# Kernel tuning notes

Measured on AMD Instinct MI355X. Metric: run time of the kernel, lower is better.

Reference implementation:

```python
import jax, jax.numpy as jnp
import numpy as np

EPS = 1e-10
BETA_SCALE = 1.0
TEMP = 0.5


def setup_inputs() -> dict:
    key = jax.random.key(0)
    ks = jax.random.split(key, 8)
    D = 128
    return {
        "root_mu_min": jax.random.normal(ks[0], (1, 64, D), dtype=jnp.float32),
        "root_mu_max": jax.random.normal(ks[1], (1, 64, D), dtype=jnp.float32),
        "root_beta_min_raw": jax.random.normal(ks[2], (1, 64, D), dtype=jnp.float32),
        "root_beta_max_raw": jax.random.normal(ks[3], (1, 64, D), dtype=jnp.float32),
        "adj_logits0": jax.random.normal(ks[4], (512, 64), dtype=jnp.float32),
        "adj_logits1": jax.random.normal(ks[5], (2048, 512), dtype=jnp.float32),
        "u0": jax.random.uniform(ks[6], (1, 512, 64), dtype=jnp.float32),
        "u1": jax.random.uniform(ks[7], (1, 2048, 512), dtype=jnp.float32),
    }


def _gumbel_sigmoid_hard(logits, u):
    # gumbel noise from externally supplied uniforms, straight-through hard threshold
    g = -jnp.log(-jnp.log(u + EPS) + EPS)
    y_soft = jax.nn.sigmoid((logits + g) / TEMP)
    y_hard = (y_soft > 0.5).astype(y_soft.dtype)
    return y_hard - jax.lax.stop_gradient(y_soft) + y_soft


def _weighted_intersection(mu_min, mu_max, beta_min, beta_max, w):
    # w: (1, C, P); parent boxes: (1, P, D)
    wsum = jnp.sum(w, axis=2)[..., None] + EPS                      # (1, C, 1)
    b_min = jnp.einsum('bcp,bpd->bcd', w, beta_min) / wsum           # (1, C, D)
    b_max = jnp.einsum('bcp,bpd->bcd', w, beta_max) / wsum           # (1, C, D)
    logw = jnp.log(w + EPS)[..., None]                               # (1, C, P, 1)
    arg_min = logw + mu_min[:, None, :, :] / b_min[:, :, None, :]    # (1, C, P, D)
    mu_min_i = b_min * jax.nn.logsumexp(arg_min, axis=2)             # (1, C, D)
    arg_max = logw - mu_max[:, None, :, :] / b_max[:, :, None, :]    # (1, C, P, D)
    mu_max_i = -b_max * jax.nn.logsumexp(arg_max, axis=2)            # (1, C, D)
    return mu_min_i, mu_max_i, b_min, b_max


def reference(root_mu_min, root_mu_max, root_beta_min_raw, root_beta_max_raw,
              adj_logits0, adj_logits1, u0, u1):
    beta_min = jax.nn.sigmoid(root_beta_min_raw) * BETA_SCALE + 1e-6
    beta_max = jax.nn.sigmoid(root_beta_max_raw) * BETA_SCALE + 1e-6
    level = (root_mu_min, root_mu_max, beta_min, beta_max)
    outs = list(level)
    for logits, u in ((adj_logits0, u0), (adj_logits1, u1)):
        w = _gumbel_sigmoid_hard(logits[None], u)  # (1, C, P)
        level = _weighted_intersection(*level, w)
        outs.extend(level)
    return tuple(outs)
```

## Files before the change

kernel.cpp:

```cpp
#include <hip/hip_runtime.h>
#include <cmath>

#define DD 128
#define LOG2E 1.4426950408889634f
#define MMARGIN 4.16f

__device__ __forceinline__ float sigm(float x) { return 1.0f / (1.0f + __expf(-x)); }

__global__ __launch_bounds__(512, 4)
void k_lvl1(const float* __restrict__ mu_min0, const float* __restrict__ mu_max0,
            const float* __restrict__ braw_min, const float* __restrict__ braw_max,
            const float* __restrict__ adj0, const float* __restrict__ u0,
            float* __restrict__ out,
            float2* __restrict__ mu2_1, float2* __restrict__ bb2_1,
            float4* __restrict__ pmaxf) {
    __shared__ float wsh[64];
    __shared__ int npres;
    __shared__ float4 red[8][64];
    __shared__ float4 cmx[8][64];
    __shared__ float4 carrA[64], carrB[64];
    const int tid = threadIdx.x;
    const int w = tid >> 6, lane = tid & 63;
    const int c = blockIdx.x;

    if (tid < 16) {
        int i = blockIdx.x * 16 + tid;
        out[i] = mu_min0[i];
        out[8192 + i] = mu_max0[i];
        out[16384 + i] = sigm(braw_min[i]) + 1e-6f;
        out[24576 + i] = sigm(braw_max[i]) + 1e-6f;
    }

    if (tid < 64) {
        int idx = c * 64 + tid;
        float uu = u0[idx] + 1e-10f;
        float g = -__logf(-__logf(uu) + 1e-10f);
        bool pres = (adj0[idx] + g) > 0.0f;
        wsh[tid] = pres ? 1.0f : 1e-10f;
        unsigned long long m = __ballot(pres);
        if (tid == 0) npres = (int)__popcll(m);
    }
    __syncthreads();

    const int p0 = w * 8;
    const int dbase = 2 * lane;

    float4 accB = make_float4(0.f, 0.f, 0.f, 0.f);
    float4 mrow[8];
    float wreg[8];
    float cm_mn0 = -INFINITY, cm_mn1 = -INFINITY, cm_ng0 = -INFINITY, cm_ng1 = -INFINITY;
    #pragma unroll
    for (int z = 0; z < 8; ++z) {
        int p = p0 + z;
        float2 bmr = *(const float2*)(braw_min + p * DD + dbase);
        float2 bxr = *(const float2*)(braw_max + p * DD + dbase);
        float2 mnr = *(const float2*)(mu_min0 + p * DD + dbase);
        float2 mxr = *(const float2*)(mu_max0 + p * DD + dbase);
        float bm0 = sigm(bmr.x) + 1e-6f, bm1 = sigm(bmr.y) + 1e-6f;
        float bx0 = sigm(bxr.x) + 1e-6f, bx1 = sigm(bxr.y) + 1e-6f;
        mrow[z] = make_float4(mnr.x, mxr.x, mnr.y, mxr.y);
        cm_mn0 = fmaxf(cm_mn0, mnr.x); cm_mn1 = fmaxf(cm_mn1, mnr.y);
        cm_ng0 = fmaxf(cm_ng0, -mxr.x); cm_ng1 = fmaxf(cm_ng1, -mxr.y);
        float wv = wsh[p];
        wreg[z] = wv;
        accB.x = fmaf(wv, bm0, accB.x);
        accB.y = fmaf(wv, bx0, accB.y);
        accB.z = fmaf(wv, bm1, accB.z);
        accB.w = fmaf(wv, bx1, accB.w);
    }
    red[w][lane] = accB;
    cmx[w][lane] = make_float4(cm_mn0, cm_ng0, cm_mn1, cm_ng1);
    __syncthreads();

    float bmin0, bmax0, bmin1, bmax1, rmin0, rmin1, nrmax0, nrmax1, Mm0, Mm1, Mg0, Mg1;
    if (tid < 64) {
        float4 S = red[0][lane];
        float4 M = cmx[0][lane];
        #pragma unroll
        for (int ww = 1; ww < 8; ++ww) {
            float4 t = red[ww][lane];
            S.x += t.x; S.y += t.y; S.z += t.z; S.w += t.w;
            float4 m = cmx[ww][lane];
            M.x = fmaxf(M.x, m.x); M.y = fmaxf(M.y, m.y);
            M.z = fmaxf(M.z, m.z); M.w = fmaxf(M.w, m.w);
        }
        Mm0 = M.x; Mg0 = M.y; Mm1 = M.z; Mg1 = M.w;
        if (c == 0) {
            pmaxf[lane] = make_float4(Mm0 + MMARGIN, Mg0 + MMARGIN,
                                      Mm1 + MMARGIN, Mg1 + MMARGIN);
        }
        const float wsv = (float)npres + 1e-10f;
        bmin0 = S.x / wsv; bmax0 = S.y / wsv; bmin1 = S.z / wsv; bmax1 = S.w / wsv;
        rmin0 = 1.0f / fmaxf(bmin0, 1e-30f);
        rmin1 = 1.0f / fmaxf(bmin1, 1e-30f);
        nrmax0 = -1.0f / fmaxf(bmax0, 1e-30f);
        nrmax1 = -1.0f / fmaxf(bmax1, 1e-30f);
        float rm20 = rmin0 * LOG2E, rm21 = rmin1 * LOG2E;
        float nx20 = nrmax0 * LOG2E, nx21 = nrmax1 * LOG2E;
        carrA[lane] = make_float4(rm20, rm21, nx20, nx21);
        carrB[lane] = make_float4(-rm20 * Mm0, -rm21 * Mm1, nx20 * Mg0, nx21 * Mg1);
    }
    __syncthreads();

    float4 cA = carrA[lane], cB = carrB[lane];

    float4 accS = make_float4(0.f, 0.f, 0.f, 0.f);
    #pragma unroll
    for (int z = 0; z < 8; ++z) {
        float4 q = mrow[z];
        float wv = wreg[z];
        accS.x = fmaf(wv, __builtin_amdgcn_exp2f(fmaf(q.x, cA.x, cB.x)), accS.x);
        accS.y = fmaf(wv, __builtin_amdgcn_exp2f(fmaf(q.y, cA.z, cB.z)), accS.y);
        accS.z = fmaf(wv, __builtin_amdgcn_exp2f(fmaf(q.z, cA.y, cB.y)), accS.z);
        accS.w = fmaf(wv, __builtin_amdgcn_exp2f(fmaf(q.w, cA.w, cB.w)), accS.w);
    }
    red[w][lane] = accS;
    __syncthreads();

    if (tid < 64) {
        float4 S = red[0][lane];
        #pragma unroll
        for (int ww = 1; ww < 8; ++ww) {
            float4 t = red[ww][lane];
            S.x += t.x; S.y += t.y; S.z += t.z; S.w += t.w;
        }
        const float S10 = fmaxf(S.x, 1e-35f);
        const float S20 = fmaxf(S.y, 1e-35f);
        const float S11 = fmaxf(S.z, 1e-35f);
        const float S21 = fmaxf(S.w, 1e-35f);
        const int idx = c * DD + 2 * lane;
        float v10 = bmin0 * fmaf(rmin0, Mm0, __logf(S10));
        float v11 = bmin1 * fmaf(rmin1, Mm1, __logf(S11));
        float v20 = -bmax0 * fmaf(-nrmax0, Mg0, __logf(S20));
        float v21 = -bmax1 * fmaf(-nrmax1, Mg1, __logf(S21));
        *(float2*)(out + 32768 + idx)  = make_float2(v10, v11);
        *(float2*)(out + 98304 + idx)  = make_float2(v20, v21);
        *(float2*)(out + 163840 + idx) = make_float2(bmin0, bmin1);
        *(float2*)(out + 229376 + idx) = make_float2(bmax0, bmax1);
        *(float4*)(mu2_1 + idx) = make_float4(v10, v20, v11, v21);
        *(float4*)(bb2_1 + idx) = make_float4(bmin0, bmax0, bmin1, bmax1);
    }
}

__global__ __launch_bounds__(512, 4)
void k_level2d(const float* __restrict__ logits, const float* __restrict__ u,
               const float2* __restrict__ bb2, const float2* __restrict__ mu2,
               const float4* __restrict__ pmaxf,
               float* __restrict__ o_mu_min, float* __restrict__ o_mu_max,
               float* __restrict__ o_b_min, float* __restrict__ o_b_max) {
    constexpr int P = 512, TC = 4;
    __shared__ __align__(16) float wsh[P][TC];
    __shared__ int npres[TC];
    __shared__ float4 red[8][TC][64];
    __shared__ float4 carrA[TC][64], carrB[TC][64];
    const int tid = threadIdx.x;
    const int w = tid >> 6;
    const int lane = tid & 63;
    const int c0 = blockIdx.x * TC;
    if (tid < TC) npres[tid] = 0;
    __syncthreads();

    #pragma unroll
    for (int it = 0; it < TC; ++it) {
        int idx = (c0 + it) * P + tid;
        float uu = u[idx] + 1e-10f;
        float g = -__logf(-__logf(uu) + 1e-10f);
        bool pres = (logits[idx] + g) > 0.0f;
        wsh[tid][it] = pres ? 1.0f : 1e-10f;
        unsigned long long m = __ballot(pres);
        if (lane == 0) atomicAdd(&npres[it], (int)__popcll(m));
    }
    __syncthreads();

    const unsigned lb = (unsigned)(lane << 4);
    const char* bbc = (const char*)bb2 + (unsigned)(w * 64) * 1024u + lb;
    const char* muc = (const char*)mu2 + (unsigned)(w * 64) * 1024u + lb;
    const int p0 = w * 64;

    float4 accB[TC];
    #pragma unroll
    for (int j = 0; j < TC; ++j) accB[j] = make_float4(0.f, 0.f, 0.f, 0.f);
    for (int z = 0; z < 64; z += 4) {
        float4 q0 = *(const float4*)(bbc + (unsigned)(z + 0) * 1024u);
        float4 q1 = *(const float4*)(bbc + (unsigned)(z + 1) * 1024u);
        float4 q2 = *(const float4*)(bbc + (unsigned)(z + 2) * 1024u);
        float4 q3 = *(const float4*)(bbc + (unsigned)(z + 3) * 1024u);
        float4 w0 = *(const float4*)wsh[p0 + z + 0];
        float4 w1 = *(const float4*)wsh[p0 + z + 1];
        float4 w2 = *(const float4*)wsh[p0 + z + 2];
        float4 w3 = *(const float4*)wsh[p0 + z + 3];
        const float* wf0 = (const float*)&w0;
        const float* wf1 = (const float*)&w1;
        const float* wf2 = (const float*)&w2;
        const float* wf3 = (const float*)&w3;
        #pragma unroll
        for (int j = 0; j < TC; ++j) {
            accB[j].x = fmaf(wf0[j], q0.x, fmaf(wf1[j], q1.x, fmaf(wf2[j], q2.x, fmaf(wf3[j], q3.x, accB[j].x))));
            accB[j].y = fmaf(wf0[j], q0.y, fmaf(wf1[j], q1.y, fmaf(wf2[j], q2.y, fmaf(wf3[j], q3.y, accB[j].y))));
            accB[j].z = fmaf(wf0[j], q0.z, fmaf(wf1[j], q1.z, fmaf(wf2[j], q2.z, fmaf(wf3[j], q3.z, accB[j].z))));
            accB[j].w = fmaf(wf0[j], q0.w, fmaf(wf1[j], q1.w, fmaf(wf2[j], q2.w, fmaf(wf3[j], q3.w, accB[j].w))));
        }
    }
    #pragma unroll
    for (int j = 0; j < TC; ++j) red[w][j][lane] = accB[j];
    __syncthreads();

    float bmin0, bmax0, bmin1, bmax1, rmin0, rmin1, nrmax0, nrmax1, Mm0, Mm1, Mg0, Mg1;
    const int rj = tid >> 6;
    if (tid < 256) {
        float4 S = red[0][rj][lane];
        #pragma unroll
        for (int ww = 1; ww < 8; ++ww) {
            float4 t = red[ww][rj][lane];
            S.x += t.x; S.y += t.y; S.z += t.z; S.w += t.w;
        }
        float4 km = pmaxf[lane];
        Mm0 = km.x; Mg0 = km.y; Mm1 = km.z; Mg1 = km.w;
        const float wsv = (float)npres[rj] + 1e-10f;
        bmin0 = S.x / wsv; bmax0 = S.y / wsv; bmin1 = S.z / wsv; bmax1 = S.w / wsv;
        rmin0 = 1.0f / fmaxf(bmin0, 1e-30f);
        rmin1 = 1.0f / fmaxf(bmin1, 1e-30f);
        nrmax0 = -1.0f / fmaxf(bmax0, 1e-30f);
        nrmax1 = -1.0f / fmaxf(bmax1, 1e-30f);
        float rm20 = rmin0 * LOG2E, rm21 = rmin1 * LOG2E;
        float nx20 = nrmax0 * LOG2E, nx21 = nrmax1 * LOG2E;
        carrA[rj][lane] = make_float4(rm20, rm21, nx20, nx21);
        carrB[rj][lane] = make_float4(-rm20 * Mm0, -rm21 * Mm1, nx20 * Mg0, nx21 * Mg1);
    }
    __syncthreads();

    float4 cA[TC], cB[TC];
    #pragma unroll
    for (int j = 0; j < TC; ++j) { cA[j] = carrA[j][lane]; cB[j] = carrB[j][lane]; }

    float4 accS[TC];
    #pragma unroll
    for (int j = 0; j < TC; ++j) accS[j] = make_float4(0.f, 0.f, 0.f, 0.f);
    for (int z = 0; z < 64; z += 4) {
        float4 q0 = *(const float4*)(muc + (unsigned)(z + 0) * 1024u);
        float4 q1 = *(const float4*)(muc + (unsigned)(z + 1) * 1024u);
        float4 q2 = *(const float4*)(muc + (unsigned)(z + 2) * 1024u);
        float4 q3 = *(const float4*)(muc + (unsigned)(z + 3) * 1024u);
        float4 w0 = *(const float4*)wsh[p0 + z + 0];
        float4 w1 = *(const float4*)wsh[p0 + z + 1];
        float4 w2 = *(const float4*)wsh[p0 + z + 2];
        float4 w3 = *(const float4*)wsh[p0 + z + 3];
        const float* wf0 = (const float*)&w0;
        const float* wf1 = (const float*)&w1;
        const float* wf2 = (const float*)&w2;
        const float* wf3 = (const float*)&w3;
        #pragma unroll
        for (int j = 0; j < TC; ++j) {
            if (wf0[j] > 0.5f) {
                accS[j].x += __builtin_amdgcn_exp2f(fmaf(q0.x, cA[j].x, cB[j].x));
                accS[j].y += __builtin_amdgcn_exp2f(fmaf(q0.y, cA[j].z, cB[j].z));
                accS[j].z += __builtin_amdgcn_exp2f(fmaf(q0.z, cA[j].y, cB[j].y));
                accS[j].w += __builtin_amdgcn_exp2f(fmaf(q0.w, cA[j].w, cB[j].w));
            }
            if (wf1[j] > 0.5f) {
                accS[j].x += __builtin_amdgcn_exp2f(fmaf(q1.x, cA[j].x, cB[j].x));
                accS[j].y += __builtin_amdgcn_exp2f(fmaf(q1.y, cA[j].z, cB[j].z));
                accS[j].z += __builtin_amdgcn_exp2f(fmaf(q1.z, cA[j].y, cB[j].y));
                accS[j].w += __builtin_amdgcn_exp2f(fmaf(q1.w, cA[j].w, cB[j].w));
            }
            if (wf2[j] > 0.5f) {
                accS[j].x += __builtin_amdgcn_exp2f(fmaf(q2.x, cA[j].x, cB[j].x));
                accS[j].y += __builtin_amdgcn_exp2f(fmaf(q2.y, cA[j].z, cB[j].z));
                accS[j].z += __builtin_amdgcn_exp2f(fmaf(q2.z, cA[j].y, cB[j].y));
                accS[j].w += __builtin_amdgcn_exp2f(fmaf(q2.w, cA[j].w, cB[j].w));
            }
            if (wf3[j] > 0.5f) {
                accS[j].x += __builtin_amdgcn_exp2f(fmaf(q3.x, cA[j].x, cB[j].x));
                accS[j].y += __builtin_amdgcn_exp2f(fmaf(q3.y, cA[j].z, cB[j].z));
                accS[j].z += __builtin_amdgcn_exp2f(fmaf(q3.z, cA[j].y, cB[j].y));
                accS[j].w += __builtin_amdgcn_exp2f(fmaf(q3.w, cA[j].w, cB[j].w));
            }
        }
    }
    #pragma unroll
    for (int j = 0; j < TC; ++j) red[w][j][lane] = accS[j];
    __syncthreads();

    if (tid < 256) {
        float4 S = red[0][rj][lane];
        #pragma unroll
        for (int ww = 1; ww < 8; ++ww) {
            float4 t = red[ww][rj][lane];
            S.x += t.x; S.y += t.y; S.z += t.z; S.w += t.w;
        }
        const float S10 = fmaxf(S.x, 1e-35f);
        const float S20 = fmaxf(S.y, 1e-35f);
        const float S11 = fmaxf(S.z, 1e-35f);
        const float S21 = fmaxf(S.w, 1e-35f);
        const int idx = (c0 + rj) * DD + 2 * lane;
        float v10 = bmin0 * fmaf(rmin0, Mm0, __logf(S10));
        float v11 = bmin1 * fmaf(rmin1, Mm1, __logf(S11));
        float v20 = -bmax0 * fmaf(-nrmax0, Mg0, __logf(S20));
        float v21 = -bmax1 * fmaf(-nrmax1, Mg1, __logf(S21));
        *(float2*)(o_mu_min + idx) = make_float2(v10, v11);
        *(float2*)(o_mu_max + idx) = make_float2(v20, v21);
        *(float2*)(o_b_min + idx)  = make_float2(bmin0, bmin1);
        *(float2*)(o_b_max + idx)  = make_float2(bmax0, bmax1);
    }
}

extern "C" void kernel_launch(void* const* d_in, const int* in_sizes, int n_in,
                              void* d_out, int out_size, void* d_ws, size_t ws_size,
                              hipStream_t stream) {
    const float* mu_min0  = (const float*)d_in[0];
    const float* mu_max0  = (const float*)d_in[1];
    const float* braw_min = (const float*)d_in[2];
    const float* braw_max = (const float*)d_in[3];
    const float* adj0     = (const float*)d_in[4];
    const float* adj1     = (const float*)d_in[5];
    const float* u0       = (const float*)d_in[6];
    const float* u1       = (const float*)d_in[7];
    float* out = (float*)d_out;
    float* ws = (float*)d_ws;

    float4* pmaxf = (float4*)ws;
    float2* mu2_1 = (float2*)(ws + 256);
    float2* bb2_1 = mu2_1 + 512 * DD;


    k_lvl1<<<dim3(512), dim3(512), 0, stream>>>(
        mu_min0, mu_max0, braw_min, braw_max, adj0, u0,
        out, mu2_1, bb2_1, pmaxf);

    k_level2d<<<dim3(512), dim3(512), 0, stream>>>(
        adj1, u1, bb2_1, mu2_1, pmaxf,
        out + 294912, out + 557056, out + 819200, out + 1081344);
}
```

Before: 114.9 us.

## Split level-2 feature dimension across two blocks with half-split parent layout

Level 1 now writes its parent box arrays in two halves of the feature dimension (64 features each), and level 2 launches twice as many blocks, each handling one half for a tile of 4 children. This halves the per-thread register and shared memory footprint, which allows a higher occupancy launch bound, and doubles the grid to fill more compute units. The cost is that every block repeats the gumbel sampling of the logits and uniforms, so those reads and log computations are done twice, and stores become scalar rather than vector.

```diff
diff --git a/kernel.cpp b/kernel.cpp
--- a/kernel.cpp
+++ b/kernel.cpp
@@ -137,12 +137,14 @@
         *(float2*)(out + 98304 + idx)  = make_float2(v20, v21);
         *(float2*)(out + 163840 + idx) = make_float2(bmin0, bmin1);
         *(float2*)(out + 229376 + idx) = make_float2(bmax0, bmax1);
-        *(float4*)(mu2_1 + idx) = make_float4(v10, v20, v11, v21);
-        *(float4*)(bb2_1 + idx) = make_float4(bmin0, bmax0, bmin1, bmax1);
+        const int h = lane >> 5;
+        const int dloc = (2 * lane) & 63;
+        *(float4*)(mu2_1 + h * 32768 + c * 64 + dloc) = make_float4(v10, v20, v11, v21);
+        *(float4*)(bb2_1 + h * 32768 + c * 64 + dloc) = make_float4(bmin0, bmax0, bmin1, bmax1);
     }
 }
 
-__global__ __launch_bounds__(512, 4)
+__global__ __launch_bounds__(512, 8)
 void k_level2d(const float* __restrict__ logits, const float* __restrict__ u,
                const float2* __restrict__ bb2, const float2* __restrict__ mu2,
                const float4* __restrict__ pmaxf,
@@ -151,12 +153,13 @@
     constexpr int P = 512, TC = 4;
     __shared__ __align__(16) float wsh[P][TC];
     __shared__ int npres[TC];
-    __shared__ float4 red[8][TC][64];
-    __shared__ float4 carrA[TC][64], carrB[TC][64];
+    __shared__ float2 red[8][TC][64];
+    __shared__ float2 carrA[TC][64], carrB[TC][64];
     const int tid = threadIdx.x;
     const int w = tid >> 6;
     const int lane = tid & 63;
-    const int c0 = blockIdx.x * TC;
+    const int h = blockIdx.x & 1;
+    const int c0 = (blockIdx.x >> 1) * TC;
     if (tid < TC) npres[tid] = 0;
     __syncthreads();
 
@@ -172,19 +175,20 @@
     }
     __syncthreads();
 
-    const unsigned lb = (unsigned)(lane << 4);
-    const char* bbc = (const char*)bb2 + (unsigned)(w * 64) * 1024u + lb;
-    const char* muc = (const char*)mu2 + (unsigned)(w * 64) * 1024u + lb;
+    const char* bbc = (const char*)bb2 + (unsigned)h * 262144u
+                      + (unsigned)(w * 64) * 512u + (unsigned)(lane << 3);
+    const char* muc = (const char*)mu2 + (unsigned)h * 262144u
+                      + (unsigned)(w * 64) * 512u + (unsigned)(lane << 3);
     const int p0 = w * 64;
 
-    float4 accB[TC];
-    #pragma unroll
-    for (int j = 0; j < TC; ++j) accB[j] = make_float4(0.f, 0.f, 0.f, 0.f);
+    float2 accB[TC];
+    #pragma unroll
+    for (int j = 0; j < TC; ++j) accB[j] = make_float2(0.f, 0.f);
     for (int z = 0; z < 64; z += 4) {
-        float4 q0 = *(const float4*)(bbc + (unsigned)(z + 0) * 1024u);
-        float4 q1 = *(const float4*)(bbc + (unsigned)(z + 1) * 1024u);
-        float4 q2 = *(const float4*)(bbc + (unsigned)(z + 2) * 1024u);
-        float4 q3 = *(const float4*)(bbc + (unsigned)(z + 3) * 1024u);
+        float2 q0 = *(const float2*)(bbc + (unsigned)(z + 0) * 512u);
+        float2 q1 = *(const float2*)(bbc + (unsigned)(z + 1) * 512u);
+        float2 q2 = *(const float2*)(bbc + (unsigned)(z + 2) * 512u);
+        float2 q3 = *(const float2*)(bbc + (unsigned)(z + 3) * 512u);
         float4 w0 = *(const float4*)wsh[p0 + z + 0];
         float4 w1 = *(const float4*)wsh[p0 + z + 1];
         float4 w2 = *(const float4*)wsh[p0 + z + 2];
@@ -197,50 +201,46 @@
         for (int j = 0; j < TC; ++j) {
             accB[j].x = fmaf(wf0[j], q0.x, fmaf(wf1[j], q1.x, fmaf(wf2[j], q2.x, fmaf(wf3[j], q3.x, accB[j].x))));
             accB[j].y = fmaf(wf0[j], q0.y, fmaf(wf1[j], q1.y, fmaf(wf2[j], q2.y, fmaf(wf3[j], q3.y, accB[j].y))));
-            accB[j].z = fmaf(wf0[j], q0.z, fmaf(wf1[j], q1.z, fmaf(wf2[j], q2.z, fmaf(wf3[j], q3.z, accB[j].z))));
-            accB[j].w = fmaf(wf0[j], q0.w, fmaf(wf1[j], q1.w, fmaf(wf2[j], q2.w, fmaf(wf3[j], q3.w, accB[j].w))));
         }
     }
     #pragma unroll
     for (int j = 0; j < TC; ++j) red[w][j][lane] = accB[j];
     __syncthreads();
 
-    float bmin0, bmax0, bmin1, bmax1, rmin0, rmin1, nrmax0, nrmax1, Mm0, Mm1, Mg0, Mg1;
+    float bmin, bmax, rmin, nrmax, Mm, Mg;
     const int rj = tid >> 6;
     if (tid < 256) {
-        float4 S = red[0][rj][lane];
+        float2 S = red[0][rj][lane];
         #pragma unroll
         for (int ww = 1; ww < 8; ++ww) {
-            float4 t = red[ww][rj][lane];
-            S.x += t.x; S.y += t.y; S.z += t.z; S.w += t.w;
-        }
-        float4 km = pmaxf[lane];
-        Mm0 = km.x; Mg0 = km.y; Mm1 = km.z; Mg1 = km.w;
+            float2 t = red[ww][rj][lane];
+            S.x += t.x; S.y += t.y;
+        }
+        float2 km = ((const float2*)pmaxf)[h * 64 + lane];
+        Mm = km.x; Mg = km.y;
         const float wsv = (float)npres[rj] + 1e-10f;
-        bmin0 = S.x / wsv; bmax0 = S.y / wsv; bmin1 = S.z / wsv; bmax1 = S.w / wsv;
-        rmin0 = 1.0f / fmaxf(bmin0, 1e-30f);
-        rmin1 = 1.0f / fmaxf(bmin1, 1e-30f);
-        nrmax0 = -1.0f / fmaxf(bmax0, 1e-30f);
-        nrmax1 = -1.0f / fmaxf(bmax1, 1e-30f);
-        float rm20 = rmin0 * LOG2E, rm21 = rmin1 * LOG2E;
-        float nx20 = nrmax0 * LOG2E, nx21 = nrmax1 * LOG2E;
-        carrA[rj][lane] = make_float4(rm20, rm21, nx20, nx21);
-        carrB[rj][lane] = make_float4(-rm20 * Mm0, -rm21 * Mm1, nx20 * Mg0, nx21 * Mg1);
-    }
-    __syncthreads();
-
-    float4 cA[TC], cB[TC];
+        bmin = S.x / wsv; bmax = S.y / wsv;
+        rmin = 1.0f / fmaxf(bmin, 1e-30f);
+        nrmax = -1.0f / fmaxf(bmax, 1e-30f);
+        float rm2 = rmin * LOG2E;
+        float nx2 = nrmax * LOG2E;
+        carrA[rj][lane] = make_float2(rm2, nx2);
+        carrB[rj][lane] = make_float2(-rm2 * Mm, nx2 * Mg);
+    }
+    __syncthreads();
+
+    float2 cA[TC], cB[TC];
     #pragma unroll
     for (int j = 0; j < TC; ++j) { cA[j] = carrA[j][lane]; cB[j] = carrB[j][lane]; }
 
-    float4 accS[TC];
-    #pragma unroll
-    for (int j = 0; j < TC; ++j) accS[j] = make_float4(0.f, 0.f, 0.f, 0.f);
+    float2 accS[TC];
+    #pragma unroll
+    for (int j = 0; j < TC; ++j) accS[j] = make_float2(0.f, 0.f);
     for (int z = 0; z < 64; z += 4) {
-        float4 q0 = *(const float4*)(muc + (unsigned)(z + 0) * 1024u);
-        float4 q1 = *(const float4*)(muc + (unsigned)(z + 1) * 1024u);
-        float4 q2 = *(const float4*)(muc + (unsigned)(z + 2) * 1024u);
-        float4 q3 = *(const float4*)(muc + (unsigned)(z + 3) * 1024u);
+        float2 q0 = *(const float2*)(muc + (unsigned)(z + 0) * 512u);
+        float2 q1 = *(const float2*)(muc + (unsigned)(z + 1) * 512u);
+        float2 q2 = *(const float2*)(muc + (unsigned)(z + 2) * 512u);
+        float2 q3 = *(const float2*)(muc + (unsigned)(z + 3) * 512u);
         float4 w0 = *(const float4*)wsh[p0 + z + 0];
         float4 w1 = *(const float4*)wsh[p0 + z + 1];
         float4 w2 = *(const float4*)wsh[p0 + z + 2];
@@ -253,27 +253,19 @@
         for (int j = 0; j < TC; ++j) {
             if (wf0[j] > 0.5f) {
                 accS[j].x += __builtin_amdgcn_exp2f(fmaf(q0.x, cA[j].x, cB[j].x));
-                accS[j].y += __builtin_amdgcn_exp2f(fmaf(q0.y, cA[j].z, cB[j].z));
-                accS[j].z += __builtin_amdgcn_exp2f(fmaf(q0.z, cA[j].y, cB[j].y));
-                accS[j].w += __builtin_amdgcn_exp2f(fmaf(q0.w, cA[j].w, cB[j].w));
+                accS[j].y += __builtin_amdgcn_exp2f(fmaf(q0.y, cA[j].y, cB[j].y));
             }
             if (wf1[j] > 0.5f) {
                 accS[j].x += __builtin_amdgcn_exp2f(fmaf(q1.x, cA[j].x, cB[j].x));
-                accS[j].y += __builtin_amdgcn_exp2f(fmaf(q1.y, cA[j].z, cB[j].z));
-                accS[j].z += __builtin_amdgcn_exp2f(fmaf(q1.z, cA[j].y, cB[j].y));
-                accS[j].w += __builtin_amdgcn_exp2f(fmaf(q1.w, cA[j].w, cB[j].w));
+                accS[j].y += __builtin_amdgcn_exp2f(fmaf(q1.y, cA[j].y, cB[j].y));
             }
             if (wf2[j] > 0.5f) {
                 accS[j].x += __builtin_amdgcn_exp2f(fmaf(q2.x, cA[j].x, cB[j].x));
-                accS[j].y += __builtin_amdgcn_exp2f(fmaf(q2.y, cA[j].z, cB[j].z));
-                accS[j].z += __builtin_amdgcn_exp2f(fmaf(q2.z, cA[j].y, cB[j].y));
-                accS[j].w += __builtin_amdgcn_exp2f(fmaf(q2.w, cA[j].w, cB[j].w));
+                accS[j].y += __builtin_amdgcn_exp2f(fmaf(q2.y, cA[j].y, cB[j].y));
             }
             if (wf3[j] > 0.5f) {
                 accS[j].x += __builtin_amdgcn_exp2f(fmaf(q3.x, cA[j].x, cB[j].x));
-                accS[j].y += __builtin_amdgcn_exp2f(fmaf(q3.y, cA[j].z, cB[j].z));
-                accS[j].z += __builtin_amdgcn_exp2f(fmaf(q3.z, cA[j].y, cB[j].y));
-                accS[j].w += __builtin_amdgcn_exp2f(fmaf(q3.w, cA[j].w, cB[j].w));
+                accS[j].y += __builtin_amdgcn_exp2f(fmaf(q3.y, cA[j].y, cB[j].y));
             }
         }
     }
@@ -282,25 +274,21 @@
     __syncthreads();
 
     if (tid < 256) {
-        float4 S = red[0][rj][lane];
+        float2 S = red[0][rj][lane];
         #pragma unroll
         for (int ww = 1; ww < 8; ++ww) {
-            float4 t = red[ww][rj][lane];
-            S.x += t.x; S.y += t.y; S.z += t.z; S.w += t.w;
-        }
-        const float S10 = fmaxf(S.x, 1e-35f);
-        const float S20 = fmaxf(S.y, 1e-35f);
-        const float S11 = fmaxf(S.z, 1e-35f);
-        const float S21 = fmaxf(S.w, 1e-35f);
-        const int idx = (c0 + rj) * DD + 2 * lane;
-        float v10 = bmin0 * fmaf(rmin0, Mm0, __logf(S10));
-        float v11 = bmin1 * fmaf(rmin1, Mm1, __logf(S11));
-        float v20 = -bmax0 * fmaf(-nrmax0, Mg0, __logf(S20));
-        float v21 = -bmax1 * fmaf(-nrmax1, Mg1, __logf(S21));
-        *(float2*)(o_mu_min + idx) = make_float2(v10, v11);
-        *(float2*)(o_mu_max + idx) = make_float2(v20, v21);
-        *(float2*)(o_b_min + idx)  = make_float2(bmin0, bmin1);
-        *(float2*)(o_b_max + idx)  = make_float2(bmax0, bmax1);
+            float2 t = red[ww][rj][lane];
+            S.x += t.x; S.y += t.y;
+        }
+        const float S1 = fmaxf(S.x, 1e-35f);
+        const float S2 = fmaxf(S.y, 1e-35f);
+        const int idx = (c0 + rj) * DD + h * 64 + lane;
+        float v1 = bmin * fmaf(rmin, Mm, __logf(S1));
+        float v2 = -bmax * fmaf(-nrmax, Mg, __logf(S2));
+        o_mu_min[idx] = v1;
+        o_mu_max[idx] = v2;
+        o_b_min[idx]  = bmin;
+        o_b_max[idx]  = bmax;
     }
 }
 
@@ -327,7 +315,7 @@
         mu_min0, mu_max0, braw_min, braw_max, adj0, u0,
         out, mu2_1, bb2_1, pmaxf);
 
-    k_level2d<<<dim3(512), dim3(512), 0, stream>>>(
+    k_level2d<<<dim3(1024), dim3(512), 0, stream>>>(
         adj1, u1, bb2_1, mu2_1, pmaxf,
         out + 294912, out + 557056, out + 819200, out + 1081344);
 }
```

New measurement: 169.9 us. 47.9% more time.
